# Performance work log

Measured on AMD Instinct MI355X. Metric: run time of the kernel, lower is better.

Reference implementation:

```python
import jax, jax.numpy as jnp
import numpy as np

D, H, W = 8, 64, 64  # image_shape
EPS = 1e-6
LOG_2PI = float(np.log(2.0 * np.pi))


def _pixel_positions():
    z = jnp.arange(D, dtype=jnp.float32) - (D - 1) / 2.0
    y = jnp.arange(H, dtype=jnp.float32) - (H - 1) / 2.0
    x = jnp.arange(W, dtype=jnp.float32) - (W - 1) / 2.0
    zg, yg, xg = jnp.meshgrid(z, y, x, indexing='ij')  # [D,H,W]
    return jnp.stack([xg, yg, zg], axis=-1).reshape(-1, 3)  # [N,3], order (x,y,z)


def setup_inputs() -> dict:
    key = jax.random.key(0)
    ks = jax.random.split(key, 5)
    return {
        'representation': jax.random.normal(ks[0], (1024, 256), dtype=jnp.float32),
        'mean_W': jax.random.normal(ks[1], (3, 256), dtype=jnp.float32) * 0.05,
        'mean_b': jax.random.normal(ks[2], (3,), dtype=jnp.float32) * 0.05,
        'scale_W': jax.random.normal(ks[3], (6, 256), dtype=jnp.float32) * 0.05,
        'scale_b': jax.random.normal(ks[4], (6,), dtype=jnp.float32) * 0.05,
    }


def reference(representation, mean_W, mean_b, scale_W, scale_b):
    # tiny projections
    means = representation @ mean_W.T + mean_b          # [B,3]
    raw = representation @ scale_W.T + scale_b          # [B,6]
    s = jax.nn.softplus(raw) + EPS                      # softplus in forward
    # FillScaleTriL: vec -> lower-tri (row-major: (0,0),(1,0),(1,1),(2,0),(2,1),(2,2)),
    # then softplus applied again to the diagonal only.
    L00 = jax.nn.softplus(s[:, 0])
    L10 = s[:, 1]
    L11 = jax.nn.softplus(s[:, 2])
    L20 = s[:, 3]
    L21 = s[:, 4]
    L22 = jax.nn.softplus(s[:, 5])

    pix = _pixel_positions()                            # [N,3]
    diff = pix[None, :, :] - means[:, None, :]          # [B,N,3]
    # hardcoded 3x3 forward-substitution: y = L^{-1} diff
    y0 = diff[..., 0] / L00[:, None]
    y1 = (diff[..., 1] - L10[:, None] * y0) / L11[:, None]
    y2 = (diff[..., 2] - L20[:, None] * y0 - L21[:, None] * y1) / L22[:, None]
    maha = y0 * y0 + y1 * y1 + y2 * y2                  # [B,N]
    log_det = jnp.log(L00) + jnp.log(L11) + jnp.log(L22)  # [B]
    log_probs = -0.5 * maha - log_det[:, None] - 1.5 * LOG_2PI  # [B,N]

    log_probs_stable = log_probs - jnp.max(log_probs, axis=1, keepdims=True)
    profile = jnp.exp(log_probs_stable)
    profile = profile / (jnp.sum(profile, axis=1, keepdims=True) + 1e-10)
    return profile
```

## Files before the change

kernel.cpp:

```cpp
#include <hip/hip_runtime.h>
#include <math.h>

#define NG    1024
#define KD    256
#define NPIX  32768
#define BLOCK 512
#define PT    64

#define C_15_LOG2PI 2.7568155996140185f

__device__ __forceinline__ float softplus_f(float x) {
    return fmaxf(x, 0.0f) + log1pf(expf(-fabsf(x)));
}

__global__ __launch_bounds__(BLOCK)
void mvn_profile_kernel(const float* __restrict__ rep,
                        const float* __restrict__ mean_W,
                        const float* __restrict__ mean_b,
                        const float* __restrict__ scale_W,
                        const float* __restrict__ scale_b,
                        float* __restrict__ out)
{
    const int g = blockIdx.x;
    const int t = threadIdx.x;

    __shared__ float s_part[9][4];
    __shared__ float s_par[10];
    __shared__ float s_red[8];

    if (t < KD) {
        float r = rep[g * KD + t];
        float acc[9];
        #pragma unroll
        for (int k = 0; k < 3; ++k) acc[k]     = r * mean_W[k * KD + t];
        #pragma unroll
        for (int k = 0; k < 6; ++k) acc[3 + k] = r * scale_W[k * KD + t];
        #pragma unroll
        for (int k = 0; k < 9; ++k) {
            float v = acc[k];
            #pragma unroll
            for (int off = 32; off >= 1; off >>= 1)
                v += __shfl_xor(v, off, 64);
            if ((t & 63) == 0) s_part[k][t >> 6] = v;
        }
    }
    __syncthreads();
    if (t == 0) {
        float dsum[9];
        #pragma unroll
        for (int k = 0; k < 9; ++k)
            dsum[k] = (s_part[k][0] + s_part[k][1]) + (s_part[k][2] + s_part[k][3]);
        float mx = dsum[0] + mean_b[0];
        float my = dsum[1] + mean_b[1];
        float mz = dsum[2] + mean_b[2];
        float s0 = softplus_f(dsum[3] + scale_b[0]) + 1e-6f;
        float s1 = softplus_f(dsum[4] + scale_b[1]) + 1e-6f;
        float s2 = softplus_f(dsum[5] + scale_b[2]) + 1e-6f;
        float s3 = softplus_f(dsum[6] + scale_b[3]) + 1e-6f;
        float s4 = softplus_f(dsum[7] + scale_b[4]) + 1e-6f;
        float s5 = softplus_f(dsum[8] + scale_b[5]) + 1e-6f;
        float L00 = softplus_f(s0);
        float L11 = softplus_f(s2);
        float L22 = softplus_f(s5);
        s_par[0] = mx; s_par[1] = my; s_par[2] = mz;
        s_par[3] = 1.0f / L00;
        s_par[4] = s1;
        s_par[5] = 1.0f / L11;
        s_par[6] = s3;
        s_par[7] = s4;
        s_par[8] = 1.0f / L22;
        s_par[9] = logf(L00) + logf(L11) + logf(L22) + C_15_LOG2PI;
    }
    __syncthreads();
    const float mx  = s_par[0], my  = s_par[1], mz  = s_par[2];
    const float r00 = s_par[3], L10 = s_par[4], r11 = s_par[5];
    const float L20 = s_par[6], L21 = s_par[7], r22 = s_par[8];
    const float c   = s_par[9];

    const float px    = (float)(t & 63) - 31.5f;
    const float y0    = (px - mx) * r00;
    const float negc2 = -(c + 0.5f * y0 * y0);
    const float dyoff = -31.5f - my - L10 * y0;
    const float dzoff = -3.5f  - mz - L20 * y0;

    float lp[PT];
    float lmax = -3.4e38f;
    const int jbase = t >> 6;
    #pragma unroll
    for (int i = 0; i < PT; ++i) {
        int   j  = jbase + 8 * i;
        float fy = (float)(j & 63);
        float fz = (float)(j >> 6);
        float y1 = (fy + dyoff) * r11;
        float w  = fz + dzoff - L21 * y1;
        float y2 = w * r22;
        float q  = y1 * y1 + y2 * y2;
        float v  = fmaf(-0.5f, q, negc2);
        lp[i] = v;
        lmax = fmaxf(lmax, v);
    }

    #pragma unroll
    for (int off = 32; off >= 1; off >>= 1)
        lmax = fmaxf(lmax, __shfl_xor(lmax, off, 64));
    if ((t & 63) == 0) s_red[t >> 6] = lmax;
    __syncthreads();
    float m = s_red[0];
    #pragma unroll
    for (int k = 1; k < 8; ++k) m = fmaxf(m, s_red[k]);

    float lsum = 0.0f;
    #pragma unroll
    for (int i = 0; i < PT; ++i) {
        float e = __expf(lp[i] - m);
        lp[i] = e;
        lsum += e;
    }
    #pragma unroll
    for (int off = 32; off >= 1; off >>= 1)
        lsum += __shfl_xor(lsum, off, 64);
    __syncthreads();
    if ((t & 63) == 0) s_red[t >> 6] = lsum;
    __syncthreads();
    float S = 0.0f;
    #pragma unroll
    for (int k = 0; k < 8; ++k) S += s_red[k];
    const float scale = 1.0f / (S + 1e-10f);

    float* op = out + (size_t)g * NPIX + t;
    #pragma unroll
    for (int i = 0; i < PT; ++i)
        op[i * BLOCK] = lp[i] * scale;
}

extern "C" void kernel_launch(void* const* d_in, const int* in_sizes, int n_in,
                              void* d_out, int out_size, void* d_ws, size_t ws_size,
                              hipStream_t stream) {
    const float* rep     = (const float*)d_in[0];
    const float* mean_W  = (const float*)d_in[1];
    const float* mean_b  = (const float*)d_in[2];
    const float* scale_W = (const float*)d_in[3];
    const float* scale_b = (const float*)d_in[4];
    float* out = (float*)d_out;

    hipLaunchKernelGGL(mvn_profile_kernel, dim3(NG), dim3(BLOCK), 0, stream,
                       rep, mean_W, mean_b, scale_W, scale_b, out);
}
```

Measured before the change: 150.7 us.

## Restructure MVN profile with float4 pixel quads, quadratic x-expansion, and single-pass softmax

Each thread now handles four adjacent x pixels over all 8 z slices with 1024 threads per block. The Mahalanobis form is expanded as a quadratic in the x offset so each extra pixel costs only a couple of FMAs plus an exp2. The max-subtraction pass and its block reduction are dropped: exponentials are computed directly with constant log terms cancelled and summed in one pass. The projections are split one dot product per wave using float4 loads, and output is written with float4 stores. Removing the max shift risks underflow, with the sum going to zero, if a Gaussian mean lies far outside the grid.

Measured after the change: 150.0 us. No clear change (-0.5%).

```diff
diff --git a/kernel.cpp b/kernel.cpp
--- a/kernel.cpp
+++ b/kernel.cpp
@@ -4,10 +4,17 @@
 #define NG    1024
 #define KD    256
 #define NPIX  32768
-#define BLOCK 512
-#define PT    64
+#define BLOCK 1024
+#define NQUAD 8
 
-#define C_15_LOG2PI 2.7568155996140185f
+#define K2C   (-0.72134752044448170f)
+#define TWOK2 (-1.44269504088896340f)
+
+#if __has_builtin(__builtin_amdgcn_exp2f)
+#define EXP2F(x) __builtin_amdgcn_exp2f(x)
+#else
+#define EXP2F(x) __expf((x) * 0.69314718055994531f)
+#endif
 
 __device__ __forceinline__ float softplus_f(float x) {
     return fmaxf(x, 0.0f) + log1pf(expf(-fabsf(x)));
@@ -21,116 +28,103 @@
                         const float* __restrict__ scale_b,
                         float* __restrict__ out)
 {
-    const int g = blockIdx.x;
-    const int t = threadIdx.x;
+    const int g    = blockIdx.x;
+    const int t    = threadIdx.x;
+    const int w    = t >> 6;
+    const int lane = t & 63;
 
-    __shared__ float s_part[9][4];
-    __shared__ float s_par[10];
-    __shared__ float s_red[8];
+    __shared__ float s_dot[9];
+    __shared__ float s_par[12];
+    __shared__ float s_red[16];
 
-    if (t < KD) {
-        float r = rep[g * KD + t];
-        float acc[9];
+    if (w < 9) {
+        const float4* r4 = (const float4*)(rep + (size_t)g * KD);
+        const float4* w4 = (w < 3) ? (const float4*)(mean_W + w * KD)
+                                   : (const float4*)(scale_W + (w - 3) * KD);
+        float4 a = r4[lane];
+        float4 b = w4[lane];
+        float acc = a.x * b.x + a.y * b.y + a.z * b.z + a.w * b.w;
         #pragma unroll
-        for (int k = 0; k < 3; ++k) acc[k]     = r * mean_W[k * KD + t];
-        #pragma unroll
-        for (int k = 0; k < 6; ++k) acc[3 + k] = r * scale_W[k * KD + t];
-        #pragma unroll
-        for (int k = 0; k < 9; ++k) {
-            float v = acc[k];
-            #pragma unroll
-            for (int off = 32; off >= 1; off >>= 1)
-                v += __shfl_xor(v, off, 64);
-            if ((t & 63) == 0) s_part[k][t >> 6] = v;
-        }
+        for (int off = 32; off >= 1; off >>= 1)
+            acc += __shfl_xor(acc, off, 64);
+        if (lane == 0) s_dot[w] = acc;
     }
     __syncthreads();
+
     if (t == 0) {
-        float dsum[9];
-        #pragma unroll
-        for (int k = 0; k < 9; ++k)
-            dsum[k] = (s_part[k][0] + s_part[k][1]) + (s_part[k][2] + s_part[k][3]);
-        float mx = dsum[0] + mean_b[0];
-        float my = dsum[1] + mean_b[1];
-        float mz = dsum[2] + mean_b[2];
-        float s0 = softplus_f(dsum[3] + scale_b[0]) + 1e-6f;
-        float s1 = softplus_f(dsum[4] + scale_b[1]) + 1e-6f;
-        float s2 = softplus_f(dsum[5] + scale_b[2]) + 1e-6f;
-        float s3 = softplus_f(dsum[6] + scale_b[3]) + 1e-6f;
-        float s4 = softplus_f(dsum[7] + scale_b[4]) + 1e-6f;
-        float s5 = softplus_f(dsum[8] + scale_b[5]) + 1e-6f;
+        float mx = s_dot[0] + mean_b[0];
+        float my = s_dot[1] + mean_b[1];
+        float mz = s_dot[2] + mean_b[2];
+        float s0 = softplus_f(s_dot[3] + scale_b[0]) + 1e-6f;
+        float s1 = softplus_f(s_dot[4] + scale_b[1]) + 1e-6f;
+        float s2 = softplus_f(s_dot[5] + scale_b[2]) + 1e-6f;
+        float s3 = softplus_f(s_dot[6] + scale_b[3]) + 1e-6f;
+        float s4 = softplus_f(s_dot[7] + scale_b[4]) + 1e-6f;
+        float s5 = softplus_f(s_dot[8] + scale_b[3 + 2]) + 1e-6f;
         float L00 = softplus_f(s0);
         float L11 = softplus_f(s2);
         float L22 = softplus_f(s5);
-        s_par[0] = mx; s_par[1] = my; s_par[2] = mz;
-        s_par[3] = 1.0f / L00;
-        s_par[4] = s1;
-        s_par[5] = 1.0f / L11;
-        s_par[6] = s3;
-        s_par[7] = s4;
-        s_par[8] = 1.0f / L22;
-        s_par[9] = logf(L00) + logf(L11) + logf(L22) + C_15_LOG2PI;
+        float r00 = 1.0f / L00;
+        float r11 = 1.0f / L11;
+        float r22 = 1.0f / L22;
+        float a1 = -s1 * r00 * r11;
+        float a2 = -(s3 * r00 + s4 * a1) * r22;
+        float R  = r00 * r00 + a1 * a1 + a2 * a2;
+        s_par[0]  = mx;  s_par[1]  = my;  s_par[2]  = mz;
+        s_par[3]  = r00; s_par[4]  = s1;  s_par[5]  = r11;
+        s_par[6]  = s3;  s_par[7]  = s4;  s_par[8]  = r22;
+        s_par[9]  = a1;  s_par[10] = a2;  s_par[11] = K2C * R;
     }
     __syncthreads();
+
     const float mx  = s_par[0], my  = s_par[1], mz  = s_par[2];
     const float r00 = s_par[3], L10 = s_par[4], r11 = s_par[5];
     const float L20 = s_par[6], L21 = s_par[7], r22 = s_par[8];
-    const float c   = s_par[9];
+    const float a1  = s_par[9], a2  = s_par[10], RK = s_par[11];
 
-    const float px    = (float)(t & 63) - 31.5f;
-    const float y0    = (px - mx) * r00;
-    const float negc2 = -(c + 0.5f * y0 * y0);
-    const float dyoff = -31.5f - my - L10 * y0;
-    const float dzoff = -3.5f  - mz - L20 * y0;
+    const float px0 = (float)((t & 15) << 2) - 31.5f;
+    const float py  = (float)(t >> 4) - 31.5f;
+    const float y0  = (px0 - mx) * r00;
+    const float y1  = (py - my - L10 * y0) * r11;
+    const float zc  = (-3.5f - mz - L20 * y0 - L21 * y1) * r22;
+    const float c0  = fmaf(y0, y0, y1 * y1);
+    const float qc  = fmaf(y0, r00, y1 * a1);
 
-    float lp[PT];
-    float lmax = -3.4e38f;
-    const int jbase = t >> 6;
+    float4 e[NQUAD];
+    float lsum = 0.0f;
     #pragma unroll
-    for (int i = 0; i < PT; ++i) {
-        int   j  = jbase + 8 * i;
-        float fy = (float)(j & 63);
-        float fz = (float)(j >> 6);
-        float y1 = (fy + dyoff) * r11;
-        float w  = fz + dzoff - L21 * y1;
-        float y2 = w * r22;
-        float q  = y1 * y1 + y2 * y2;
-        float v  = fmaf(-0.5f, q, negc2);
-        lp[i] = v;
-        lmax = fmaxf(lmax, v);
+    for (int i = 0; i < NQUAD; ++i) {
+        float y2 = fmaf((float)i, r22, zc);
+        float P  = fmaf(y2, y2, c0);
+        float Q  = fmaf(y2, a2, qc);
+        float kP = K2C * P;
+        float QK = TWOK2 * Q;
+        float4 v;
+        v.x = EXP2F(kP);
+        v.y = EXP2F(fmaf(1.0f, fmaf(1.0f, RK, QK), kP));
+        v.z = EXP2F(fmaf(2.0f, fmaf(2.0f, RK, QK), kP));
+        v.w = EXP2F(fmaf(3.0f, fmaf(3.0f, RK, QK), kP));
+        e[i] = v;
+        lsum += ((v.x + v.y) + (v.z + v.w));
     }
 
     #pragma unroll
     for (int off = 32; off >= 1; off >>= 1)
-        lmax = fmaxf(lmax, __shfl_xor(lmax, off, 64));
-    if ((t & 63) == 0) s_red[t >> 6] = lmax;
-    __syncthreads();
-    float m = s_red[0];
-    #pragma unroll
-    for (int k = 1; k < 8; ++k) m = fmaxf(m, s_red[k]);
-
-    float lsum = 0.0f;
-    #pragma unroll
-    for (int i = 0; i < PT; ++i) {
-        float e = __expf(lp[i] - m);
-        lp[i] = e;
-        lsum += e;
-    }
-    #pragma unroll
-    for (int off = 32; off >= 1; off >>= 1)
         lsum += __shfl_xor(lsum, off, 64);
-    __syncthreads();
-    if ((t & 63) == 0) s_red[t >> 6] = lsum;
+    if (lane == 0) s_red[w] = lsum;
     __syncthreads();
     float S = 0.0f;
     #pragma unroll
-    for (int k = 0; k < 8; ++k) S += s_red[k];
+    for (int k = 0; k < 16; ++k) S += s_red[k];
     const float scale = 1.0f / (S + 1e-10f);
 
-    float* op = out + (size_t)g * NPIX + t;
+    float4* op = (float4*)(out + (size_t)g * NPIX) + t;
     #pragma unroll
-    for (int i = 0; i < PT; ++i)
-        op[i * BLOCK] = lp[i] * scale;
+    for (int i = 0; i < NQUAD; ++i) {
+        float4 v = e[i];
+        v.x *= scale; v.y *= scale; v.z *= scale; v.w *= scale;
+        op[i * BLOCK] = v;
+    }
 }
 
 extern "C" void kernel_launch(void* const* d_in, const int* in_sizes, int n_in,
```
